# Kernel tuning notes

Measured on AMD Instinct MI355X. Metric: run time of the kernel, lower is better.

Reference implementation:

```python
import jax, jax.numpy as jnp
import numpy as np
import math

T = 120      # frame_num == audio_len == max_seq_len
D = 64       # hidden_layer_size
H = 2        # n_head
DH = D // H
DFF = 2 * D
DOUT = 31
PERIOD = 10
EPS = 1e-5
NEG = -1e9
SCALE = 1.0 / math.sqrt(DH)
SLOPES = (1.0 / 16.0, 1.0 / 256.0)  # ALiBi slopes for n_head=2


def _pe():
    # PeriodicPositionalEncoding: sinusoid over one period, tiled
    pos = jnp.arange(PERIOD, dtype=jnp.float32)[:, None]
    div = jnp.exp(jnp.arange(0, D, 2, dtype=jnp.float32) * (-math.log(10000.0) / D))
    s, c = jnp.sin(pos * div), jnp.cos(pos * div)
    pe = jnp.stack([s, c], axis=-1).reshape(PERIOD, D)  # interleave sin/cos
    return jnp.tile(pe, (T // PERIOD + 1, 1))[:T]


def _alibi_mask():
    # causal mask + ALiBi bias: alibi[i,j] = -slope * floor((i-j)/period) for j<=i
    slopes = jnp.array(SLOPES, dtype=jnp.float32)
    i = jnp.arange(T)[:, None]
    j = jnp.arange(T)[None, :]
    rel = ((i - j) // PERIOD).astype(jnp.float32)
    return jnp.where(j <= i, -slopes[:, None, None] * rel, NEG)  # [H,T,T]


def _ln(x, g, b):
    m = x.mean(-1, keepdims=True)
    v = ((x - m) ** 2).mean(-1, keepdims=True)
    return (x - m) / jnp.sqrt(v + EPS) * g + b


def setup_inputs() -> dict:
    key = jax.random.key(0)
    ks = iter(jax.random.split(key, 32))
    n = lambda shape, s=0.05: jax.random.normal(next(ks), shape, dtype=jnp.float32) * s
    inp = {
        'audio': jax.random.normal(next(ks), (1, T, 1024), dtype=jnp.float32),
        'W_audio': n((D, 1024)), 'b_audio': n((D,)),
        'obj_W': n((D, 5)),
        'Wq': n((D, D)), 'bq': n((D,)), 'Wk': n((D, D)), 'bk': n((D,)),
        'Wv': n((D, D)), 'bv': n((D,)), 'Wo': n((D, D)), 'bo': n((D,)),
        'Wv2': n((D, D)), 'bv2': n((D,)), 'Wo2': n((D, D)), 'bo2': n((D,)),
        'g1': jnp.ones((D,)), 'be1': jnp.zeros((D,)),
        'g2': jnp.ones((D,)), 'be2': jnp.zeros((D,)),
        'g3': jnp.ones((D,)), 'be3': jnp.zeros((D,)),
        'W1': n((DFF, D)), 'c1': n((DFF,)), 'W2': n((D, DFF)), 'c2': n((D,)),
        'Wr': n((DOUT, D)), 'br': n((DOUT,)), 'Wm': n((D, DOUT)), 'bm': n((D,)),
    }
    return inp


def _forward(audio, W_audio, b_audio, obj_W, Wq, bq, Wk, bk, Wv, bv, Wo, bo,
             Wv2, bv2, Wo2, bo2, g1, be1, g2, be2, g3, be3,
             W1, c1, W2, c2, Wr, br, Wm, bm):
    mem = audio[0] @ W_audio.T + b_audio          # [S,D], S == T
    style = obj_W[:, 0]                            # obj_vector @ [1,0,0,0,0]
    pe = _pe()
    mask = _alibi_mask()
    slopes = jnp.array(SLOPES, dtype=jnp.float32)
    jarr = jnp.arange(T)

    # enc_dec_mask leaves exactly one memory key per target row (anti-diagonal
    # from the end); the feedback row t at step t always attends memory[-1],
    # so its cross-attn output is just the projected value of the last frame.
    cross_last = (mem[-1] @ Wv2.T + bv2) @ Wo2.T + bo2  # [D]

    def step(emb, t):
        # decode only the last row (row t) of the growing sequence; 1-layer
        # post-norm decoder => row t depends only on input rows 0..t.
        x = emb + pe                                 # PPE over prefix
        xq = jnp.take(x, t, axis=0)                  # [D]
        q = (xq @ Wq.T + bq).reshape(H, DH)
        k = (x @ Wk.T + bk).reshape(T, H, DH)
        v = (x @ Wv.T + bv).reshape(T, H, DH)
        bias = jnp.where(jarr <= t,
                         -slopes[:, None] * ((t - jarr) // PERIOD).astype(jnp.float32),
                         NEG)                        # [H,T]
        sc = jnp.einsum('hd,shd->hs', q, k) * SCALE + bias
        a = jax.nn.softmax(sc, axis=-1)
        sa = jnp.einsum('hs,shd->hd', a, v).reshape(D) @ Wo.T + bo
        h1 = _ln(xq + sa, g1, be1)
        h2 = _ln(h1 + cross_last, g2, be2)
        h3 = _ln(h2 + jax.nn.relu(h2 @ W1.T + c1) @ W2.T + c2, g3, be3)
        new = (h3 @ Wr.T + br) @ Wm.T + bm + style   # vertice_map(vertice_map_r(.)) + style
        emb = jax.lax.dynamic_update_slice(emb, new[None, :], (t + 1, 0))
        return emb, None

    emb0 = jnp.zeros((T, D), audio.dtype).at[0].set(style)
    emb, _ = jax.lax.scan(step, emb0, jnp.arange(T - 1))

    # final full-length decode (last loop iteration of the torch module)
    x = emb + pe
    q = (x @ Wq.T + bq).reshape(T, H, DH)
    k = (x @ Wk.T + bk).reshape(T, H, DH)
    v = (x @ Wv.T + bv).reshape(T, H, DH)
    sc = jnp.einsum('thd,shd->hts', q, k) * SCALE + mask
    a = jax.nn.softmax(sc, axis=-1)
    sa = jnp.einsum('hts,shd->thd', a, v).reshape(T, D) @ Wo.T + bo
    h1 = _ln(x + sa, g1, be1)
    # at length T with S == T the enc_dec_mask aligns target row j <-> memory row j
    cross = (mem @ Wv2.T + bv2) @ Wo2.T + bo2
    h2 = _ln(h1 + cross, g2, be2)
    h3 = _ln(h2 + jax.nn.relu(h2 @ W1.T + c1) @ W2.T + c2, g3, be3)
    return (h3 @ Wr.T + br)[None]                    # [1,T,31]


def reference(audio, W_audio, b_audio, obj_W, Wq, bq, Wk, bk, Wv, bv, Wo, bo,
              Wv2, bv2, Wo2, bo2, g1, be1, g2, be2, g3, be3,
              W1, c1, W2, c2, Wr, br, Wm, bm):
    return _forward(audio, W_audio, b_audio, obj_W, Wq, bq, Wk, bk, Wv, bv, Wo, bo,
                    Wv2, bv2, Wo2, bo2, g1, be1, g2, be2, g3, be3,
                    W1, c1, W2, c2, Wr, br, Wm, bm)
```

## Files before the change

kernel.cpp:

```cpp
#include <hip/hip_runtime.h>

typedef unsigned short u16;
typedef unsigned int   u32;
typedef _Float16 f16;
typedef f16 h2 __attribute__((ext_vector_type(2)));
typedef f16 h4 __attribute__((ext_vector_type(4)));
typedef f16 h8 __attribute__((ext_vector_type(8)));

#define T_    120
#define D_    64
#define DOUT_ 31
#define KROW_ 68
#define VROW_ 132

#if defined(__has_builtin)
#if __has_builtin(__builtin_amdgcn_fdot2)
#define DOT2(a,b,c) __builtin_amdgcn_fdot2((a),(b),(c),false)
#endif
#endif
#ifndef DOT2
#define DOT2(a,b,c) ((float)(a).x*(float)(b).x + ((float)(a).y*(float)(b).y + (c)))
#endif
#define SHV(x,i,j) __builtin_shufflevector((x),(x),(i),(j))

__device__ __forceinline__ h2 pk(float a, float b){
#if defined(__has_builtin) && __has_builtin(__builtin_amdgcn_cvt_pkrtz)
  return __builtin_bit_cast(h2, __builtin_amdgcn_cvt_pkrtz(a, b));
#else
  h2 r; r.x = (f16)a; r.y = (f16)b; return r;
#endif
}
__device__ __forceinline__ float b2f(u16 u){ return __uint_as_float(((u32)u) << 16); }
__device__ __forceinline__ float2 bp2(u32 u){
  float2 r; r.x = __uint_as_float(u << 16); r.y = __uint_as_float(u & 0xffff0000u); return r;
}
__device__ __forceinline__ u16 f2bu(float f){
  u32 u = __float_as_uint(f);
  u32 r = u + 0x7fffu + ((u >> 16) & 1u);
  return (u16)(r >> 16);
}
__device__ __forceinline__ u16 f2h16(float x){
  f16 v = (f16)x; u16 r; __builtin_memcpy(&r, &v, 2); return r;
}
#define WSYNC() do{ __asm__ __volatile__("" ::: "memory"); __builtin_amdgcn_wave_barrier(); }while(0)

__device__ __forceinline__ float dpp_sum(float x){
  int t;
  t = __builtin_amdgcn_update_dpp(0, __float_as_int(x), 0x111, 0xf, 0xf, true); x += __int_as_float(t);
  t = __builtin_amdgcn_update_dpp(0, __float_as_int(x), 0x112, 0xf, 0xf, true); x += __int_as_float(t);
  t = __builtin_amdgcn_update_dpp(0, __float_as_int(x), 0x114, 0xf, 0xf, true); x += __int_as_float(t);
  t = __builtin_amdgcn_update_dpp(0, __float_as_int(x), 0x118, 0xf, 0xf, true); x += __int_as_float(t);
  t = __builtin_amdgcn_update_dpp(0, __float_as_int(x), 0x142, 0xf, 0xf, true); x += __int_as_float(t);
  t = __builtin_amdgcn_update_dpp(0, __float_as_int(x), 0x143, 0xf, 0xf, true); x += __int_as_float(t);
  return __int_as_float(__builtin_amdgcn_readlane(__float_as_int(x), 63));
}
__device__ __forceinline__ float dpp_max_pos(float x){
  int t;
  t = __builtin_amdgcn_update_dpp(0, __float_as_int(x), 0x111, 0xf, 0xf, true); x = fmaxf(x, __int_as_float(t));
  t = __builtin_amdgcn_update_dpp(0, __float_as_int(x), 0x112, 0xf, 0xf, true); x = fmaxf(x, __int_as_float(t));
  t = __builtin_amdgcn_update_dpp(0, __float_as_int(x), 0x114, 0xf, 0xf, true); x = fmaxf(x, __int_as_float(t));
  t = __builtin_amdgcn_update_dpp(0, __float_as_int(x), 0x118, 0xf, 0xf, true); x = fmaxf(x, __int_as_float(t));
  t = __builtin_amdgcn_update_dpp(0, __float_as_int(x), 0x142, 0xf, 0xf, true); x = fmaxf(x, __int_as_float(t));
  t = __builtin_amdgcn_update_dpp(0, __float_as_int(x), 0x143, 0xf, 0xf, true); x = fmaxf(x, __int_as_float(t));
  return __int_as_float(__builtin_amdgcn_readlane(__float_as_int(x), 63));
}
__device__ __forceinline__ float pe_val(int row, int i){
  const float coef = -0.28782313662425574f;
  int p = row % 10;
  float dv  = __expf((float)(i >> 1) * coef);
  float ang = (float)p * dv;
  return (i & 1) ? __cosf(ang) : __sinf(ang);
}
__device__ __forceinline__ void loadrow32(h2* dst, const float* row){
  #pragma unroll
  for (int r = 0; r < 16; ++r){
    float4 f = ((const float4*)row)[r];
    dst[2*r]   = pk(f.x, f.y);
    dst[2*r+1] = pk(f.z, f.w);
  }
}

__global__ __launch_bounds__(256) void k_pre(const float* __restrict__ audio,
                                             const float* __restrict__ Wa, const float* __restrict__ ba,
                                             const float* __restrict__ Wv2, const float* __restrict__ bv2,
                                             const float* __restrict__ Wo2, const float* __restrict__ bo2,
                                             const float* __restrict__ Wo, const float* __restrict__ W1,
                                             const float* __restrict__ W2, const float* __restrict__ Wr,
                                             const float* __restrict__ Wm, const float* __restrict__ br,
                                             const float* __restrict__ bm,
                                             float* __restrict__ cross, float* __restrict__ Ms,
                                             float* __restrict__ bMv,
                                             u16* __restrict__ wob, u16* __restrict__ w1b,
                                             u16* __restrict__ w2b, u16* __restrict__ wrb){
  const int b = blockIdx.x, tid = threadIdx.x;
  if (b == 120){
    for (int i = tid; i < 4096; i += 256) wob[i] = f2bu(Wo[i]);
    for (int i = tid; i < 8192; i += 256){ w1b[i] = f2bu(W1[i]); w2b[i] = f2bu(W2[i]); }
    for (int i = tid; i < 1984; i += 256) wrb[i] = f2bu(Wr[i]);
    for (int idx = tid; idx < 4096; idx += 256){
      int d = idx >> 6, e = idx & 63;
      float acc = 0.f;
      #pragma unroll
      for (int j = 0; j < 31; ++j) acc += Wm[d*31 + j] * Wr[j*64 + e];
      Ms[idx] = acc;
    }
    if (tid < 64){
      float acc = bm[tid];
      #pragma unroll
      for (int j = 0; j < 31; ++j) acc += Wm[tid*31 + j] * br[j];
      bMv[tid] = acc;
    }
    return;
  }
  __shared__ float ash[1024];
  __shared__ float msh[64], tsh[64];
  for (int i = tid; i < 1024; i += 256) ash[i] = audio[b*1024 + i];
  __syncthreads();
  const int w = tid >> 6, lane = tid & 63;
  for (int d = w*16; d < w*16 + 16; ++d){
    const float4* row = (const float4*)(Wa + d*1024);
    float acc = 0.f;
    #pragma unroll
    for (int m = 0; m < 4; ++m){
      float4 wp = row[lane + 64*m];
      int j = 4*(lane + 64*m);
      acc += wp.x*ash[j] + wp.y*ash[j+1] + wp.z*ash[j+2] + wp.w*ash[j+3];
    }
    acc = dpp_sum(acc);
    if (lane == 0) msh[d] = acc + ba[d];
  }
  __syncthreads();
  if (tid < 64){
    const float4* r1 = (const float4*)(Wv2 + tid*64);
    float a = bv2[tid];
    #pragma unroll
    for (int j = 0; j < 16; ++j){ float4 p = r1[j]; a += p.x*msh[4*j] + p.y*msh[4*j+1] + p.z*msh[4*j+2] + p.w*msh[4*j+3]; }
    tsh[tid] = a;
  }
  __syncthreads();
  if (tid < 64){
    const float4* r2 = (const float4*)(Wo2 + tid*64);
    float c = bo2[tid];
    #pragma unroll
    for (int j = 0; j < 16; ++j){ float4 p = r2[j]; c += p.x*tsh[4*j] + p.y*tsh[4*j+1] + p.z*tsh[4*j+2] + p.w*tsh[4*j+3]; }
    cross[b*64 + tid] = c;
  }
}

__global__ __launch_bounds__(128, 1) void k_scan(
    const float* __restrict__ objW,
    const float* __restrict__ Wq, const float* __restrict__ bq,
    const float* __restrict__ Wk, const float* __restrict__ bk,
    const float* __restrict__ Wv, const float* __restrict__ bv,
    const float* __restrict__ Wo, const float* __restrict__ bo,
    const float* __restrict__ g1, const float* __restrict__ be1,
    const float* __restrict__ g2, const float* __restrict__ be2,
    const float* __restrict__ g3, const float* __restrict__ be3,
    const float* __restrict__ W1, const float* __restrict__ c1,
    const float* __restrict__ W2, const float* __restrict__ c2,
    const float* __restrict__ Ms, const float* __restrict__ bMv,
    const float* __restrict__ cross,
    u16* __restrict__ xw16, u16* __restrict__ Kw16, u16* __restrict__ Vw16)
{
  __shared__ __align__(16) f16 KcS[128*KROW_];
  __shared__ __align__(16) f16 VcS[D_*VROW_];
  __shared__ __align__(16) f16 xwS[T_*D_];
  __shared__ __align__(16) f16 sch[256];
  __shared__ __align__(16) f16 xh[64], qh[64], ath[64], h2h[64], h3h[64];
  __shared__ __align__(16) h2  fsh2[64];
  __shared__ float xf[64], h2f[64];
  __shared__ float pe_tab[640];

  const int tid = threadIdx.x;
  const int i = tid & 63;
  const bool w0 = tid < 64;

  h2 R0[32], R1[32], R2[32], R3[32], R4[32];
  float bA=0.f, bB=0.f, c1a=0.f, c1b=0.f, c2r=0.f, bmst=0.f, cls_r=0.f;
  float g1r=0.f,b1r=0.f,g2r=0.f,b2r=0.f,g3r=0.f,b3r=0.f;

  if (w0){
    loadrow32(R0, Wv + i*64);
    loadrow32(R1, Wo + i*64);
    loadrow32(R2, W1 + i*64);
    loadrow32(R3, W1 + (64+i)*64);
    bA = bv[i]; bB = bo[i]; c1a = c1[i]; c1b = c1[64+i];
    g1r = g1[i]; b1r = be1[i]; g2r = g2[i]; b2r = be2[i];
    cls_r = cross[119*64 + i];
  } else {
    loadrow32(R0, Wq + i*64);
    loadrow32(R1, Wk + i*64);
    {
      const float4* ra = (const float4*)(W2 + i*128);
      const float4* rb = (const float4*)(W2 + i*128 + 64);
      #pragma unroll
      for (int r = 0; r < 8; ++r){
        float4 a = ra[r], b = rb[r];
        R2[4*r+0] = pk(a.x, b.x); R2[4*r+1] = pk(a.y, b.y);
        R2[4*r+2] = pk(a.z, b.z); R2[4*r+3] = pk(a.w, b.w);
      }
      #pragma unroll
      for (int r = 0; r < 8; ++r){
        float4 a = ra[8+r], b = rb[8+r];
        R3[4*r+0] = pk(a.x, b.x); R3[4*r+1] = pk(a.y, b.y);
        R3[4*r+2] = pk(a.z, b.z); R3[4*r+3] = pk(a.w, b.w);
      }
    }
    loadrow32(R4, Ms + i*64);
    bA = bq[i]; bB = bk[i]; c2r = c2[i];
    g3r = g3[i]; b3r = be3[i];
    bmst = bMv[i] + objW[i*5];
  }
  { u32* p = (u32*)KcS; for (int idx = tid; idx < 128*KROW_/2; idx += 128) p[idx] = 0; }
  { u32* p = (u32*)VcS; for (int idx = tid; idx < D_*VROW_/2;  idx += 128) p[idx] = 0; }
  for (int idx = tid; idx < 640; idx += 128) pe_tab[idx] = pe_val(idx >> 6, idx & 63);
  __syncthreads();

  if (!w0){
    float st = objW[i*5];
    float x0 = st + pe_val(0, i);
    xf[i] = x0; xh[i] = (f16)x0; xwS[i] = (f16)x0;
    WSYNC();
    const h8* xv = (const h8*)xh;
    float q0=bA,q1=0.f,q2=0.f,q3=0.f, k0=bB,k1=0.f,k2=0.f,k3=0.f;
    #pragma unroll
    for (int r = 0; r < 8; ++r){
      h8 x = xv[r];
      h2 xa=SHV(x,0,1), xb=SHV(x,2,3), xc=SHV(x,4,5), xd=SHV(x,6,7);
      q0 = DOT2(R0[4*r+0], xa, q0); q1 = DOT2(R0[4*r+1], xb, q1);
      q2 = DOT2(R0[4*r+2], xc, q2); q3 = DOT2(R0[4*r+3], xd, q3);
      k0 = DOT2(R1[4*r+0], xa, k0); k1 = DOT2(R1[4*r+1], xb, k1);
      k2 = DOT2(R1[4*r+2], xc, k2); k3 = DOT2(R1[4*r+3], xd, k3);
    }
    qh[i] = (f16)((q0+q1)+(q2+q3));
    KcS[i] = (f16)((k0+k1)+(k2+k3));
  }

  int pp = 1;
  for (int t = 0; t < T_-1; ++t){
    __syncthreads();
    if (w0){
      {
        const h8* xv = (const h8*)xh;
        float v0=bA,v1=0.f,v2=0.f,v3=0.f;
        #pragma unroll
        for (int r = 0; r < 8; ++r){
          h8 x = xv[r];
          v0 = DOT2(R0[4*r+0], SHV(x,0,1), v0);
          v1 = DOT2(R0[4*r+1], SHV(x,2,3), v1);
          v2 = DOT2(R0[4*r+2], SHV(x,4,5), v2);
          v3 = DOT2(R0[4*r+3], SHV(x,6,7), v3);
        }
        VcS[i*VROW_ + t] = (f16)((v0+v1)+(v2+v3));
      }
      WSYNC();
      {
        const h8* qv  = (const h8*)qh;
        const h4* kr0 = (const h4*)(KcS + i*KROW_);
        const h4* kr1 = (const h4*)(KcS + (i+64)*KROW_);
        float d00a=0.f,d00b=0.f,d01a=0.f,d01b=0.f,d10a=0.f,d10b=0.f,d11a=0.f,d11b=0.f;
        #pragma unroll
        for (int r = 0; r < 4; ++r){
          h8 ql = qv[r], qhn = qv[4+r];
          h2 ql0=SHV(ql,0,1),  ql1=SHV(ql,2,3),  ql2=SHV(ql,4,5),  ql3=SHV(ql,6,7);
          h2 qh0=SHV(qhn,0,1), qh1=SHV(qhn,2,3), qh2=SHV(qhn,4,5), qh3=SHV(qhn,6,7);
          h4 ka = kr0[2*r],   kb = kr0[2*r+1];
          h4 kc = kr0[8+2*r], kd = kr0[9+2*r];
          h4 ke = kr1[2*r],   kf = kr1[2*r+1];
          h4 kg = kr1[8+2*r], kh = kr1[9+2*r];
          d00a = DOT2(SHV(ka,0,1), ql0, d00a); d00b = DOT2(SHV(ka,2,3), ql1, d00b);
          d00a = DOT2(SHV(kb,0,1), ql2, d00a); d00b = DOT2(SHV(kb,2,3), ql3, d00b);
          d10a = DOT2(SHV(kc,0,1), qh0, d10a); d10b = DOT2(SHV(kc,2,3), qh1, d10b);
          d10a = DOT2(SHV(kd,0,1), qh2, d10a); d10b = DOT2(SHV(kd,2,3), qh3, d10b);
          d01a = DOT2(SHV(ke,0,1), ql0, d01a); d01b = DOT2(SHV(ke,2,3), ql1, d01b);
          d01a = DOT2(SHV(kf,0,1), ql2, d01a); d01b = DOT2(SHV(kf,2,3), ql3, d01b);
          d11a = DOT2(SHV(kg,0,1), qh0, d11a); d11b = DOT2(SHV(kg,2,3), qh1, d11b);
          d11a = DOT2(SHV(kh,0,1), qh2, d11a); d11b = DOT2(SHV(kh,2,3), qh3, d11b);
        }
        const float SC = 0.17677669529663687f;
        int r0 = (t - i) / 10, r1 = (t - i - 64) / 10;
        bool m0 = (i <= t), m1 = (i + 64 <= t);
        float e00 = m0 ? __expf((d00a+d00b)*SC - 0.0625f*(float)r0)     : 0.f;
        float e01 = m1 ? __expf((d01a+d01b)*SC - 0.0625f*(float)r1)     : 0.f;
        float e10 = m0 ? __expf((d10a+d10b)*SC - 0.00390625f*(float)r0) : 0.f;
        float e11 = m1 ? __expf((d11a+d11b)*SC - 0.00390625f*(float)r1) : 0.f;
        float inv0 = 1.f / dpp_sum(e00 + e01);
        float inv1 = 1.f / dpp_sum(e10 + e11);
        sch[i]        = (f16)(e00*inv0);
        sch[64+i]     = (f16)(e01*inv0);
        sch[128+i]    = (f16)(e10*inv1);
        sch[192+i]    = (f16)(e11*inv1);
      }
      WSYNC();
      {
        const h8* av = (const h8*)(sch + (i >> 5)*128);
        const h4* vv = (const h4*)(VcS + i*VROW_);
        float p0=0.f,p1=0.f,p2=0.f,p3=0.f;
        #pragma unroll
        for (int r = 0; r < 15; ++r){
          h8 a = av[r];
          h4 va = vv[2*r], vb = vv[2*r+1];
          p0 = DOT2(SHV(va,0,1), SHV(a,0,1), p0);
          p1 = DOT2(SHV(va,2,3), SHV(a,2,3), p1);
          p2 = DOT2(SHV(vb,0,1), SHV(a,4,5), p2);
          p3 = DOT2(SHV(vb,2,3), SHV(a,6,7), p3);
        }
        ath[i] = (f16)((p0+p1)+(p2+p3));
      }
      WSYNC();
      {
        const h8* av = (const h8*)ath;
        float a0=bB, a1=0.f, a2=0.f, a3=0.f;
        #pragma unroll
        for (int r = 0; r < 8; ++r){
          h8 x = av[r];
          a0 = DOT2(R1[4*r+0], SHV(x,0,1), a0);
          a1 = DOT2(R1[4*r+1], SHV(x,2,3), a1);
          a2 = DOT2(R1[4*r+2], SHV(x,4,5), a2);
          a3 = DOT2(R1[4*r+3], SHV(x,6,7), a3);
        }
        float y = xf[i] + (a0+a1)+(a2+a3);
        float s = dpp_sum(y), s2 = dpp_sum(y*y);
        float m = s*(1.f/64.f), var = fmaxf(s2*(1.f/64.f) - m*m, 0.f);
        float h1 = (y - m)*rsqrtf(var + 1e-5f)*g1r + b1r;
        float z = h1 + cls_r;
        float sz = dpp_sum(z), sz2 = dpp_sum(z*z);
        float mz = sz*(1.f/64.f), vz = fmaxf(sz2*(1.f/64.f) - mz*mz, 0.f);
        float h2v = (z - mz)*rsqrtf(vz + 1e-5f)*g2r + b2r;
        h2h[i] = (f16)h2v;
        h2f[i] = h2v;
      }
      WSYNC();
      {
        const h8* hv = (const h8*)h2h;
        float a0=c1a, a1=0.f, a2=0.f, a3=0.f, b0=c1b, b1=0.f, b2=0.f, b3=0.f;
        #pragma unroll
        for (int r = 0; r < 8; ++r){
          h8 x = hv[r];
          h2 xa=SHV(x,0,1), xb=SHV(x,2,3), xc=SHV(x,4,5), xd=SHV(x,6,7);
          a0 = DOT2(R2[4*r+0], xa, a0); a1 = DOT2(R2[4*r+1], xb, a1);
          a2 = DOT2(R2[4*r+2], xc, a2); a3 = DOT2(R2[4*r+3], xd, a3);
          b0 = DOT2(R3[4*r+0], xa, b0); b1 = DOT2(R3[4*r+1], xb, b1);
          b2 = DOT2(R3[4*r+2], xc, b2); b3 = DOT2(R3[4*r+3], xd, b3);
        }
        fsh2[i] = pk(fmaxf((a0+a1)+(a2+a3), 0.f), fmaxf((b0+b1)+(b2+b3), 0.f));
      }
    }
    __syncthreads();
    if (!w0){
      float h3v;
      {
        const h8* fv = (const h8*)fsh2;
        float a0=c2r, a1=0.f, a2=0.f, a3=0.f;
        #pragma unroll
        for (int r = 0; r < 8; ++r){
          h8 x = fv[r];
          a0 = DOT2(R2[4*r+0], SHV(x,0,1), a0);
          a1 = DOT2(R2[4*r+1], SHV(x,2,3), a1);
          a2 = DOT2(R2[4*r+2], SHV(x,4,5), a2);
          a3 = DOT2(R2[4*r+3], SHV(x,6,7), a3);
        }
        #pragma unroll
        for (int r = 0; r < 8; ++r){
          h8 x = fv[8+r];
          a0 = DOT2(R3[4*r+0], SHV(x,0,1), a0);
          a1 = DOT2(R3[4*r+1], SHV(x,2,3), a1);
          a2 = DOT2(R3[4*r+2], SHV(x,4,5), a2);
          a3 = DOT2(R3[4*r+3], SHV(x,6,7), a3);
        }
        float y = h2f[i] + (a0+a1)+(a2+a3);
        float s = dpp_sum(y), s2 = dpp_sum(y*y);
        float m = s*(1.f/64.f), var = fmaxf(s2*(1.f/64.f) - m*m, 0.f);
        h3v = (y - m)*rsqrtf(var + 1e-5f)*g3r + b3r;
        h3h[i] = (f16)h3v;
      }
      WSYNC();
      {
        const h8* hv3 = (const h8*)h3h;
        float m0=bmst, m1=0.f, m2=0.f, m3=0.f;
        #pragma unroll
        for (int r = 0; r < 8; ++r){
          h8 x = hv3[r];
          m0 = DOT2(R4[4*r+0], SHV(x,0,1), m0);
          m1 = DOT2(R4[4*r+1], SHV(x,2,3), m1);
          m2 = DOT2(R4[4*r+2], SHV(x,4,5), m2);
          m3 = DOT2(R4[4*r+3], SHV(x,6,7), m3);
        }
        float xn = (m0+m1)+(m2+m3) + pe_tab[pp*64 + i];
        xf[i] = xn;
        xh[i] = (f16)xn;
        xwS[(t+1)*64 + i] = (f16)xn;
      }
      WSYNC();
      {
        const h8* xv = (const h8*)xh;
        float q0=bA,q1=0.f,q2=0.f,q3=0.f, k0=bB,k1=0.f,k2=0.f,k3=0.f;
        #pragma unroll
        for (int r = 0; r < 8; ++r){
          h8 x = xv[r];
          h2 xa=SHV(x,0,1), xb=SHV(x,2,3), xc=SHV(x,4,5), xd=SHV(x,6,7);
          q0 = DOT2(R0[4*r+0], xa, q0); q1 = DOT2(R0[4*r+1], xb, q1);
          q2 = DOT2(R0[4*r+2], xc, q2); q3 = DOT2(R0[4*r+3], xd, q3);
          k0 = DOT2(R1[4*r+0], xa, k0); k1 = DOT2(R1[4*r+1], xb, k1);
          k2 = DOT2(R1[4*r+2], xc, k2); k3 = DOT2(R1[4*r+3], xd, k3);
        }
        qh[i] = (f16)((q0+q1)+(q2+q3));
        KcS[(t+1)*KROW_ + i] = (f16)((k0+k1)+(k2+k3));
      }
    }
    pp = (pp == 9) ? 0 : pp + 1;
  }
  __syncthreads();
  if (w0){
    const h8* xv = (const h8*)xh;
    float v0=bA,v1=0.f,v2=0.f,v3=0.f;
    #pragma unroll
    for (int r = 0; r < 8; ++r){
      h8 x = xv[r];
      v0 = DOT2(R0[4*r+0], SHV(x,0,1), v0);
      v1 = DOT2(R0[4*r+1], SHV(x,2,3), v1);
      v2 = DOT2(R0[4*r+2], SHV(x,4,5), v2);
      v3 = DOT2(R0[4*r+3], SHV(x,6,7), v3);
    }
    Vw16[119*64 + i] = f2h16((v0+v1)+(v2+v3));
  }
  {
    const u16* kc = (const u16*)KcS;
    const u16* vc = (const u16*)VcS;
    for (int idx = tid; idx < 120*64; idx += 128){
      int t_ = idx >> 6, d = idx & 63;
      Kw16[idx] = kc[t_*KROW_ + d];
    }
    for (int idx = tid; idx < 119*64; idx += 128){
      int t_ = idx >> 6, d = idx & 63;
      Vw16[idx] = vc[d*VROW_ + t_];
    }
    const u32* xs32 = (const u32*)xwS;
    for (int idx = tid; idx < T_*D_/2; idx += 128) ((u32*)xw16)[idx] = xs32[idx];
  }
}

__global__ __launch_bounds__(128) void k_final(
    const float* __restrict__ Wq, const float* __restrict__ bq, const float* __restrict__ bo,
    const float* __restrict__ g1, const float* __restrict__ be1,
    const float* __restrict__ g2, const float* __restrict__ be2,
    const float* __restrict__ g3, const float* __restrict__ be3,
    const float* __restrict__ c1, const float* __restrict__ c2, const float* __restrict__ br,
    const u16* __restrict__ wo_b, const u16* __restrict__ w1_b,
    const u16* __restrict__ w2_b, const u16* __restrict__ wr_b,
    const float* __restrict__ cross, const u16* __restrict__ xw16,
    const u16* __restrict__ Kw16, const u16* __restrict__ Vw16,
    float* __restrict__ out)
{
  __shared__ float xs[64], qs[64], at[64], h2s[64], h3s[64], fs[128], sc[256];
  const int irow = blockIdx.x, tid = threadIdx.x;
  const f16* xp = (const f16*)xw16;
  const f16* kp = (const f16*)Kw16;
  const f16* vp = (const f16*)Vw16;
  if (tid < 64) xs[tid] = (float)xp[irow*64 + tid];
  __syncthreads();
  if (tid < 64){
// ... 105 lines not shown
  const float* Wo   =(const float*)d_in[10];
  const float* bo   =(const float*)d_in[11];
  const float* Wv2  =(const float*)d_in[12];
  const float* bv2  =(const float*)d_in[13];
  const float* Wo2  =(const float*)d_in[14];
  const float* bo2  =(const float*)d_in[15];
  const float* g1   =(const float*)d_in[16];
  const float* be1  =(const float*)d_in[17];
  const float* g2   =(const float*)d_in[18];
  const float* be2  =(const float*)d_in[19];
  const float* g3   =(const float*)d_in[20];
  const float* be3  =(const float*)d_in[21];
  const float* W1   =(const float*)d_in[22];
  const float* c1   =(const float*)d_in[23];
  const float* W2   =(const float*)d_in[24];
  const float* c2   =(const float*)d_in[25];
  const float* Wr   =(const float*)d_in[26];
  const float* br   =(const float*)d_in[27];
  const float* Wm   =(const float*)d_in[28];
  const float* bm   =(const float*)d_in[29];

  float* ws    = (float*)d_ws;
  float* cross = ws;
  float* Ms    = ws + 7680;
  float* bMv   = ws + 11776;
  u16* xw16 = (u16*)(ws + 11840);
  u16* Kw16 = xw16 + 7680;
  u16* Vw16 = Kw16 + 7680;
  u16* wo_b = Vw16 + 7680;
  u16* w1_b = wo_b + 4096;
  u16* w2_b = w1_b + 8192;
  u16* wr_b = w2_b + 8192;
  float* out = (float*)d_out;

  k_pre  <<<dim3(121), dim3(256), 0, stream>>>(audio, Wa, ba, Wv2, bv2, Wo2, bo2,
                                               Wo, W1, W2, Wr, Wm, br, bm,
                                               cross, Ms, bMv, wo_b, w1_b, w2_b, wr_b);
  k_scan <<<dim3(1),   dim3(128), 0, stream>>>(objW, Wq, bq, Wk, bk, Wv, bv, Wo, bo,
                                               g1, be1, g2, be2, g3, be3,
                                               W1, c1, W2, c2, Ms, bMv,
                                               cross, xw16, Kw16, Vw16);
  k_final<<<dim3(120), dim3(128), 0, stream>>>(Wq, bq, bo, g1, be1, g2, be2, g3, be3,
                                               c1, c2, br, wo_b, w1_b, w2_b, wr_b,
                                               cross, xw16, Kw16, Vw16, out);
}
```

Measured before the change: 411.4 us.

## Fold output-map into QKV weights and run scan as single wave

Precomputes the composed matrices Wq·M, Wk·M, Wv·M and the per-phase bias vectors (including positional encoding) in the prep kernel. The serial scan can then produce next q/k/v/x directly from h3 in one fused matvec stage instead of computing x and then projecting it. The scan drops from two waves with __syncthreads to a single 64-thread wave using only wave barriers, with some weights moved from registers to LDS. The aim is to shorten the serial per-step dependency chain and remove block-level sync, at the cost of more precompute in the prep kernel, LDS weight reads and small fp16 rounding differences.

After: 563.9 us. 37.1% more time.

```diff
diff --git a/kernel.cpp b/kernel.cpp
--- a/kernel.cpp
+++ b/kernel.cpp
@@ -12,6 +12,7 @@
 #define DOUT_ 31
 #define KROW_ 68
 #define VROW_ 132
+#define WP_   68
 
 #if defined(__has_builtin)
 #if __has_builtin(__builtin_amdgcn_fdot2)
@@ -30,7 +31,6 @@
   h2 r; r.x = (f16)a; r.y = (f16)b; return r;
 #endif
 }
-__device__ __forceinline__ float b2f(u16 u){ return __uint_as_float(((u32)u) << 16); }
 __device__ __forceinline__ float2 bp2(u32 u){
   float2 r; r.x = __uint_as_float(u << 16); r.y = __uint_as_float(u & 0xffff0000u); return r;
 }
@@ -38,9 +38,6 @@
   u32 u = __float_as_uint(f);
   u32 r = u + 0x7fffu + ((u >> 16) & 1u);
   return (u16)(r >> 16);
-}
-__device__ __forceinline__ u16 f2h16(float x){
-  f16 v = (f16)x; u16 r; __builtin_memcpy(&r, &v, 2); return r;
 }
 #define WSYNC() do{ __asm__ __volatile__("" ::: "memory"); __builtin_amdgcn_wave_barrier(); }while(0)
 
@@ -87,13 +84,25 @@
                                              const float* __restrict__ Wo, const float* __restrict__ W1,
                                              const float* __restrict__ W2, const float* __restrict__ Wr,
                                              const float* __restrict__ Wm, const float* __restrict__ br,
-                                             const float* __restrict__ bm,
-                                             float* __restrict__ cross, float* __restrict__ Ms,
-                                             float* __restrict__ bMv,
+                                             const float* __restrict__ bm, const float* __restrict__ objW,
+                                             const float* __restrict__ Wq, const float* __restrict__ bq,
+                                             const float* __restrict__ Wk, const float* __restrict__ bk,
+                                             const float* __restrict__ Wv, const float* __restrict__ bv,
+                                             float* __restrict__ cross,
+                                             float* __restrict__ Mw,  float* __restrict__ QMw,
+                                             float* __restrict__ KMw, float* __restrict__ VMw,
+                                             float* __restrict__ qbw, float* __restrict__ kbw,
+                                             float* __restrict__ vbw, float* __restrict__ xbw,
+                                             float* __restrict__ q0w, float* __restrict__ k0w,
+                                             float* __restrict__ v0w, float* __restrict__ x0w,
                                              u16* __restrict__ wob, u16* __restrict__ w1b,
                                              u16* __restrict__ w2b, u16* __restrict__ wrb){
   const int b = blockIdx.x, tid = threadIdx.x;
   if (b == 120){
+    __shared__ float Msh[4096];
+    __shared__ float bMs[64];
+    __shared__ float uS[640];
+    __shared__ float x0s[64];
     for (int i = tid; i < 4096; i += 256) wob[i] = f2bu(Wo[i]);
     for (int i = tid; i < 8192; i += 256){ w1b[i] = f2bu(W1[i]); w2b[i] = f2bu(W2[i]); }
     for (int i = tid; i < 1984; i += 256) wrb[i] = f2bu(Wr[i]);
@@ -102,13 +111,50 @@
       float acc = 0.f;
       #pragma unroll
       for (int j = 0; j < 31; ++j) acc += Wm[d*31 + j] * Wr[j*64 + e];
-      Ms[idx] = acc;
+      Msh[idx] = acc; Mw[idx] = acc;
     }
     if (tid < 64){
       float acc = bm[tid];
       #pragma unroll
       for (int j = 0; j < 31; ++j) acc += Wm[tid*31 + j] * br[j];
-      bMv[tid] = acc;
+      bMs[tid] = acc + objW[tid*5];
+      x0s[tid] = objW[tid*5] + pe_val(0, tid);
+    }
+    __syncthreads();
+    for (int idx = tid; idx < 640; idx += 256){
+      int p = idx >> 6, d = idx & 63;
+      float u = bMs[d] + pe_val(p, d);
+      uS[idx] = u; xbw[idx] = u;
+    }
+    __syncthreads();
+    for (int idx = tid; idx < 4096; idx += 256){
+      int d = idx >> 6, e = idx & 63;
+      float aq = 0.f, ak = 0.f, av = 0.f;
+      #pragma unroll
+      for (int j = 0; j < 64; ++j){
+        float m = Msh[j*64 + e];
+        aq += Wq[d*64 + j]*m; ak += Wk[d*64 + j]*m; av += Wv[d*64 + j]*m;
+      }
+      QMw[idx] = aq; KMw[idx] = ak; VMw[idx] = av;
+    }
+    for (int idx = tid; idx < 640; idx += 256){
+      int p = idx >> 6, d = idx & 63;
+      float aq = bq[d], ak = bk[d], av = bv[d];
+      #pragma unroll
+      for (int j = 0; j < 64; ++j){
+        float u = uS[p*64 + j];
+        aq += Wq[d*64 + j]*u; ak += Wk[d*64 + j]*u; av += Wv[d*64 + j]*u;
+      }
+      qbw[idx] = aq; kbw[idx] = ak; vbw[idx] = av;
+    }
+    if (tid < 64){
+      float aq = bq[tid], ak = bk[tid], av = bv[tid];
+      #pragma unroll
+      for (int j = 0; j < 64; ++j){
+        float x = x0s[j];
+        aq += Wq[tid*64 + j]*x; ak += Wk[tid*64 + j]*x; av += Wv[tid*64 + j]*x;
+      }
+      q0w[tid] = aq; k0w[tid] = ak; v0w[tid] = av; x0w[tid] = x0s[tid];
     }
     return;
   }
@@ -147,296 +193,235 @@
   }
 }
 
-__global__ __launch_bounds__(128, 1) void k_scan(
-    const float* __restrict__ objW,
-    const float* __restrict__ Wq, const float* __restrict__ bq,
-    const float* __restrict__ Wk, const float* __restrict__ bk,
-    const float* __restrict__ Wv, const float* __restrict__ bv,
+__global__ __launch_bounds__(64, 1) void k_scan(
     const float* __restrict__ Wo, const float* __restrict__ bo,
+    const float* __restrict__ W1, const float* __restrict__ c1,
+    const float* __restrict__ W2, const float* __restrict__ c2,
     const float* __restrict__ g1, const float* __restrict__ be1,
     const float* __restrict__ g2, const float* __restrict__ be2,
     const float* __restrict__ g3, const float* __restrict__ be3,
-    const float* __restrict__ W1, const float* __restrict__ c1,
-    const float* __restrict__ W2, const float* __restrict__ c2,
-    const float* __restrict__ Ms, const float* __restrict__ bMv,
+    const float* __restrict__ Mw,  const float* __restrict__ QMw,
+    const float* __restrict__ KMw, const float* __restrict__ VMw,
+    const float* __restrict__ qbw, const float* __restrict__ kbw,
+    const float* __restrict__ vbw, const float* __restrict__ xbw,
+    const float* __restrict__ q0w, const float* __restrict__ k0w,
+    const float* __restrict__ v0w, const float* __restrict__ x0w,
     const float* __restrict__ cross,
     u16* __restrict__ xw16, u16* __restrict__ Kw16, u16* __restrict__ Vw16)
 {
   __shared__ __align__(16) f16 KcS[128*KROW_];
   __shared__ __align__(16) f16 VcS[D_*VROW_];
   __shared__ __align__(16) f16 xwS[T_*D_];
+  __shared__ __align__(16) f16 W1bS[D_*WP_];
+  __shared__ __align__(16) f16 W2aS[D_*WP_];
+  __shared__ __align__(16) f16 W2bS[D_*WP_];
+  __shared__ __align__(16) f16 MS[D_*WP_];
+  __shared__ float qbS[640], kbS[640], vbS[640], xbS[640];
   __shared__ __align__(16) f16 sch[256];
-  __shared__ __align__(16) f16 xh[64], qh[64], ath[64], h2h[64], h3h[64];
-  __shared__ __align__(16) h2  fsh2[64];
-  __shared__ float xf[64], h2f[64];
-  __shared__ float pe_tab[640];
-
-  const int tid = threadIdx.x;
-  const int i = tid & 63;
-  const bool w0 = tid < 64;
-
-  h2 R0[32], R1[32], R2[32], R3[32], R4[32];
-  float bA=0.f, bB=0.f, c1a=0.f, c1b=0.f, c2r=0.f, bmst=0.f, cls_r=0.f;
-  float g1r=0.f,b1r=0.f,g2r=0.f,b2r=0.f,g3r=0.f,b3r=0.f;
-
-  if (w0){
-    loadrow32(R0, Wv + i*64);
-    loadrow32(R1, Wo + i*64);
-    loadrow32(R2, W1 + i*64);
-    loadrow32(R3, W1 + (64+i)*64);
-    bA = bv[i]; bB = bo[i]; c1a = c1[i]; c1b = c1[64+i];
-    g1r = g1[i]; b1r = be1[i]; g2r = g2[i]; b2r = be2[i];
-    cls_r = cross[119*64 + i];
-  } else {
-    loadrow32(R0, Wq + i*64);
-    loadrow32(R1, Wk + i*64);
-    {
-      const float4* ra = (const float4*)(W2 + i*128);
-      const float4* rb = (const float4*)(W2 + i*128 + 64);
-      #pragma unroll
-      for (int r = 0; r < 8; ++r){
-        float4 a = ra[r], b = rb[r];
-        R2[4*r+0] = pk(a.x, b.x); R2[4*r+1] = pk(a.y, b.y);
-        R2[4*r+2] = pk(a.z, b.z); R2[4*r+3] = pk(a.w, b.w);
-      }
-      #pragma unroll
-      for (int r = 0; r < 8; ++r){
-        float4 a = ra[8+r], b = rb[8+r];
-        R3[4*r+0] = pk(a.x, b.x); R3[4*r+1] = pk(a.y, b.y);
-        R3[4*r+2] = pk(a.z, b.z); R3[4*r+3] = pk(a.w, b.w);
-      }
-    }
-    loadrow32(R4, Ms + i*64);
-    bA = bq[i]; bB = bk[i]; c2r = c2[i];
-    g3r = g3[i]; b3r = be3[i];
-    bmst = bMv[i] + objW[i*5];
-  }
-  { u32* p = (u32*)KcS; for (int idx = tid; idx < 128*KROW_/2; idx += 128) p[idx] = 0; }
-  { u32* p = (u32*)VcS; for (int idx = tid; idx < D_*VROW_/2;  idx += 128) p[idx] = 0; }
-  for (int idx = tid; idx < 640; idx += 128) pe_tab[idx] = pe_val(idx >> 6, idx & 63);
-  __syncthreads();
-
-  if (!w0){
-    float st = objW[i*5];
-    float x0 = st + pe_val(0, i);
-    xf[i] = x0; xh[i] = (f16)x0; xwS[i] = (f16)x0;
-    WSYNC();
-    const h8* xv = (const h8*)xh;
-    float q0=bA,q1=0.f,q2=0.f,q3=0.f, k0=bB,k1=0.f,k2=0.f,k3=0.f;
-    #pragma unroll
-    for (int r = 0; r < 8; ++r){
-      h8 x = xv[r];
-      h2 xa=SHV(x,0,1), xb=SHV(x,2,3), xc=SHV(x,4,5), xd=SHV(x,6,7);
-      q0 = DOT2(R0[4*r+0], xa, q0); q1 = DOT2(R0[4*r+1], xb, q1);
-      q2 = DOT2(R0[4*r+2], xc, q2); q3 = DOT2(R0[4*r+3], xd, q3);
-      k0 = DOT2(R1[4*r+0], xa, k0); k1 = DOT2(R1[4*r+1], xb, k1);
-      k2 = DOT2(R1[4*r+2], xc, k2); k3 = DOT2(R1[4*r+3], xd, k3);
-    }
-    qh[i] = (f16)((q0+q1)+(q2+q3));
-    KcS[i] = (f16)((k0+k1)+(k2+k3));
-  }
+  __shared__ __align__(16) f16 qh[64], ath[64], h2h[64], h3h[64];
+  __shared__ __align__(16) f16 fsh[128];
+
+  const int i = threadIdx.x;
+
+  h2 QM[32], KM[32], VM[32], WOr[32], W1a[32];
+  loadrow32(QM,  QMw + i*64);
+  loadrow32(KM,  KMw + i*64);
+  loadrow32(VM,  VMw + i*64);
+  loadrow32(WOr, Wo  + i*64);
+  loadrow32(W1a, W1  + i*64);
+  const float bo_r = bo[i], c1a = c1[i], c1b = c1[64+i], c2r = c2[i];
+  const float g1r = g1[i], b1r = be1[i], g2r = g2[i], b2r = be2[i], g3r = g3[i], b3r = be3[i];
+  const float cls_r = cross[119*64 + i];
+
+  for (int idx = i; idx < 4096; idx += 64){
+    int r = idx >> 6, c = idx & 63;
+    W1bS[r*WP_ + c] = (f16)W1[(64+r)*64 + c];
+    W2aS[r*WP_ + c] = (f16)W2[r*128 + c];
+    W2bS[r*WP_ + c] = (f16)W2[r*128 + 64 + c];
+    MS  [r*WP_ + c] = (f16)Mw[r*64 + c];
+  }
+  for (int idx = i; idx < 640; idx += 64){
+    qbS[idx] = qbw[idx]; kbS[idx] = kbw[idx]; vbS[idx] = vbw[idx]; xbS[idx] = xbw[idx];
+  }
+  { u32* p = (u32*)KcS; for (int idx = i; idx < 128*KROW_/2; idx += 64) p[idx] = 0; }
+  { u32* p = (u32*)VcS; for (int idx = i; idx < D_*VROW_/2;  idx += 64) p[idx] = 0; }
+  float xr = x0w[i];
+  qh[i] = (f16)q0w[i];
+  KcS[i] = (f16)k0w[i];
+  VcS[i*VROW_] = (f16)v0w[i];
+  xwS[i] = (f16)xr;
+  WSYNC();
 
   int pp = 1;
   for (int t = 0; t < T_-1; ++t){
-    __syncthreads();
-    if (w0){
-      {
-        const h8* xv = (const h8*)xh;
-        float v0=bA,v1=0.f,v2=0.f,v3=0.f;
-        #pragma unroll
-        for (int r = 0; r < 8; ++r){
-          h8 x = xv[r];
-          v0 = DOT2(R0[4*r+0], SHV(x,0,1), v0);
-          v1 = DOT2(R0[4*r+1], SHV(x,2,3), v1);
-          v2 = DOT2(R0[4*r+2], SHV(x,4,5), v2);
-          v3 = DOT2(R0[4*r+3], SHV(x,6,7), v3);
-        }
-        VcS[i*VROW_ + t] = (f16)((v0+v1)+(v2+v3));
-      }
-      WSYNC();
-      {
-        const h8* qv  = (const h8*)qh;
-        const h4* kr0 = (const h4*)(KcS + i*KROW_);
-        const h4* kr1 = (const h4*)(KcS + (i+64)*KROW_);
-        float d00a=0.f,d00b=0.f,d01a=0.f,d01b=0.f,d10a=0.f,d10b=0.f,d11a=0.f,d11b=0.f;
-        #pragma unroll
-        for (int r = 0; r < 4; ++r){
-          h8 ql = qv[r], qhn = qv[4+r];
-          h2 ql0=SHV(ql,0,1),  ql1=SHV(ql,2,3),  ql2=SHV(ql,4,5),  ql3=SHV(ql,6,7);
-          h2 qh0=SHV(qhn,0,1), qh1=SHV(qhn,2,3), qh2=SHV(qhn,4,5), qh3=SHV(qhn,6,7);
-          h4 ka = kr0[2*r],   kb = kr0[2*r+1];
-          h4 kc = kr0[8+2*r], kd = kr0[9+2*r];
-          h4 ke = kr1[2*r],   kf = kr1[2*r+1];
-          h4 kg = kr1[8+2*r], kh = kr1[9+2*r];
-          d00a = DOT2(SHV(ka,0,1), ql0, d00a); d00b = DOT2(SHV(ka,2,3), ql1, d00b);
-          d00a = DOT2(SHV(kb,0,1), ql2, d00a); d00b = DOT2(SHV(kb,2,3), ql3, d00b);
-          d10a = DOT2(SHV(kc,0,1), qh0, d10a); d10b = DOT2(SHV(kc,2,3), qh1, d10b);
-          d10a = DOT2(SHV(kd,0,1), qh2, d10a); d10b = DOT2(SHV(kd,2,3), qh3, d10b);
-          d01a = DOT2(SHV(ke,0,1), ql0, d01a); d01b = DOT2(SHV(ke,2,3), ql1, d01b);
-          d01a = DOT2(SHV(kf,0,1), ql2, d01a); d01b = DOT2(SHV(kf,2,3), ql3, d01b);
-          d11a = DOT2(SHV(kg,0,1), qh0, d11a); d11b = DOT2(SHV(kg,2,3), qh1, d11b);
-          d11a = DOT2(SHV(kh,0,1), qh2, d11a); d11b = DOT2(SHV(kh,2,3), qh3, d11b);
-        }
-        const float SC = 0.17677669529663687f;
-        int r0 = (t - i) / 10, r1 = (t - i - 64) / 10;
-        bool m0 = (i <= t), m1 = (i + 64 <= t);
-        float e00 = m0 ? __expf((d00a+d00b)*SC - 0.0625f*(float)r0)     : 0.f;
-        float e01 = m1 ? __expf((d01a+d01b)*SC - 0.0625f*(float)r1)     : 0.f;
-        float e10 = m0 ? __expf((d10a+d10b)*SC - 0.00390625f*(float)r0) : 0.f;
-        float e11 = m1 ? __expf((d11a+d11b)*SC - 0.00390625f*(float)r1) : 0.f;
-        float inv0 = 1.f / dpp_sum(e00 + e01);
-        float inv1 = 1.f / dpp_sum(e10 + e11);
-        sch[i]        = (f16)(e00*inv0);
-        sch[64+i]     = (f16)(e01*inv0);
-        sch[128+i]    = (f16)(e10*inv1);
-        sch[192+i]    = (f16)(e11*inv1);
-      }
-      WSYNC();
-      {
-        const h8* av = (const h8*)(sch + (i >> 5)*128);
-        const h4* vv = (const h4*)(VcS + i*VROW_);
-        float p0=0.f,p1=0.f,p2=0.f,p3=0.f;
-        #pragma unroll
-        for (int r = 0; r < 15; ++r){
-          h8 a = av[r];
-          h4 va = vv[2*r], vb = vv[2*r+1];
-          p0 = DOT2(SHV(va,0,1), SHV(a,0,1), p0);
-          p1 = DOT2(SHV(va,2,3), SHV(a,2,3), p1);
-          p2 = DOT2(SHV(vb,0,1), SHV(a,4,5), p2);
-          p3 = DOT2(SHV(vb,2,3), SHV(a,6,7), p3);
-        }
-        ath[i] = (f16)((p0+p1)+(p2+p3));
-      }
-      WSYNC();
-      {
-        const h8* av = (const h8*)ath;
-        float a0=bB, a1=0.f, a2=0.f, a3=0.f;
-        #pragma unroll
-        for (int r = 0; r < 8; ++r){
-          h8 x = av[r];
-          a0 = DOT2(R1[4*r+0], SHV(x,0,1), a0);
-          a1 = DOT2(R1[4*r+1], SHV(x,2,3), a1);
-          a2 = DOT2(R1[4*r+2], SHV(x,4,5), a2);
-          a3 = DOT2(R1[4*r+3], SHV(x,6,7), a3);
-        }
-        float y = xf[i] + (a0+a1)+(a2+a3);
-        float s = dpp_sum(y), s2 = dpp_sum(y*y);
-        float m = s*(1.f/64.f), var = fmaxf(s2*(1.f/64.f) - m*m, 0.f);
-        float h1 = (y - m)*rsqrtf(var + 1e-5f)*g1r + b1r;
-        float z = h1 + cls_r;
-        float sz = dpp_sum(z), sz2 = dpp_sum(z*z);
-        float mz = sz*(1.f/64.f), vz = fmaxf(sz2*(1.f/64.f) - mz*mz, 0.f);
-        float h2v = (z - mz)*rsqrtf(vz + 1e-5f)*g2r + b2r;
-        h2h[i] = (f16)h2v;
-        h2f[i] = h2v;
-      }
-      WSYNC();
-      {
-        const h8* hv = (const h8*)h2h;
-        float a0=c1a, a1=0.f, a2=0.f, a3=0.f, b0=c1b, b1=0.f, b2=0.f, b3=0.f;
-        #pragma unroll
-        for (int r = 0; r < 8; ++r){
-          h8 x = hv[r];
-          h2 xa=SHV(x,0,1), xb=SHV(x,2,3), xc=SHV(x,4,5), xd=SHV(x,6,7);
-          a0 = DOT2(R2[4*r+0], xa, a0); a1 = DOT2(R2[4*r+1], xb, a1);
-          a2 = DOT2(R2[4*r+2], xc, a2); a3 = DOT2(R2[4*r+3], xd, a3);
-          b0 = DOT2(R3[4*r+0], xa, b0); b1 = DOT2(R3[4*r+1], xb, b1);
-          b2 = DOT2(R3[4*r+2], xc, b2); b3 = DOT2(R3[4*r+3], xd, b3);
-        }
-        fsh2[i] = pk(fmaxf((a0+a1)+(a2+a3), 0.f), fmaxf((b0+b1)+(b2+b3), 0.f));
-      }
-    }
-    __syncthreads();
-    if (!w0){
-      float h3v;
-      {
-        const h8* fv = (const h8*)fsh2;
-        float a0=c2r, a1=0.f, a2=0.f, a3=0.f;
-        #pragma unroll
-        for (int r = 0; r < 8; ++r){
-          h8 x = fv[r];
-          a0 = DOT2(R2[4*r+0], SHV(x,0,1), a0);
-          a1 = DOT2(R2[4*r+1], SHV(x,2,3), a1);
-          a2 = DOT2(R2[4*r+2], SHV(x,4,5), a2);
-          a3 = DOT2(R2[4*r+3], SHV(x,6,7), a3);
-        }
-        #pragma unroll
-        for (int r = 0; r < 8; ++r){
-          h8 x = fv[8+r];
-          a0 = DOT2(R3[4*r+0], SHV(x,0,1), a0);
-          a1 = DOT2(R3[4*r+1], SHV(x,2,3), a1);
-          a2 = DOT2(R3[4*r+2], SHV(x,4,5), a2);
-          a3 = DOT2(R3[4*r+3], SHV(x,6,7), a3);
-        }
-        float y = h2f[i] + (a0+a1)+(a2+a3);
-        float s = dpp_sum(y), s2 = dpp_sum(y*y);
-        float m = s*(1.f/64.f), var = fmaxf(s2*(1.f/64.f) - m*m, 0.f);
-        h3v = (y - m)*rsqrtf(var + 1e-5f)*g3r + b3r;
-        h3h[i] = (f16)h3v;
-      }
-      WSYNC();
-      {
-        const h8* hv3 = (const h8*)h3h;
-        float m0=bmst, m1=0.f, m2=0.f, m3=0.f;
-        #pragma unroll
-        for (int r = 0; r < 8; ++r){
-          h8 x = hv3[r];
-          m0 = DOT2(R4[4*r+0], SHV(x,0,1), m0);
-          m1 = DOT2(R4[4*r+1], SHV(x,2,3), m1);
-          m2 = DOT2(R4[4*r+2], SHV(x,4,5), m2);
-          m3 = DOT2(R4[4*r+3], SHV(x,6,7), m3);
-        }
-        float xn = (m0+m1)+(m2+m3) + pe_tab[pp*64 + i];
-        xf[i] = xn;
-        xh[i] = (f16)xn;
-        xwS[(t+1)*64 + i] = (f16)xn;
-      }
-      WSYNC();
-      {
-        const h8* xv = (const h8*)xh;
-        float q0=bA,q1=0.f,q2=0.f,q3=0.f, k0=bB,k1=0.f,k2=0.f,k3=0.f;
-        #pragma unroll
-        for (int r = 0; r < 8; ++r){
-          h8 x = xv[r];
-          h2 xa=SHV(x,0,1), xb=SHV(x,2,3), xc=SHV(x,4,5), xd=SHV(x,6,7);
-          q0 = DOT2(R0[4*r+0], xa, q0); q1 = DOT2(R0[4*r+1], xb, q1);
-          q2 = DOT2(R0[4*r+2], xc, q2); q3 = DOT2(R0[4*r+3], xd, q3);
-          k0 = DOT2(R1[4*r+0], xa, k0); k1 = DOT2(R1[4*r+1], xb, k1);
-          k2 = DOT2(R1[4*r+2], xc, k2); k3 = DOT2(R1[4*r+3], xd, k3);
-        }
-        qh[i] = (f16)((q0+q1)+(q2+q3));
-        KcS[(t+1)*KROW_ + i] = (f16)((k0+k1)+(k2+k3));
-      }
-    }
+    {
+      const h8* qv  = (const h8*)qh;
+      const h4* kr0 = (const h4*)(KcS + i*KROW_);
+      const h4* kr1 = (const h4*)(KcS + (i+64)*KROW_);
+      float d00a=0.f,d00b=0.f,d01a=0.f,d01b=0.f,d10a=0.f,d10b=0.f,d11a=0.f,d11b=0.f;
+      #pragma unroll
+      for (int r = 0; r < 4; ++r){
+        h8 ql = qv[r], qhn = qv[4+r];
+        h2 ql0=SHV(ql,0,1),  ql1=SHV(ql,2,3),  ql2=SHV(ql,4,5),  ql3=SHV(ql,6,7);
+        h2 qh0=SHV(qhn,0,1), qh1=SHV(qhn,2,3), qh2=SHV(qhn,4,5), qh3=SHV(qhn,6,7);
+        h4 ka = kr0[2*r],   kb = kr0[2*r+1];
+        h4 kc = kr0[8+2*r], kd = kr0[9+2*r];
+        h4 ke = kr1[2*r],   kf = kr1[2*r+1];
+        h4 kg = kr1[8+2*r], kh = kr1[9+2*r];
+        d00a = DOT2(SHV(ka,0,1), ql0, d00a); d00b = DOT2(SHV(ka,2,3), ql1, d00b);
+        d00a = DOT2(SHV(kb,0,1), ql2, d00a); d00b = DOT2(SHV(kb,2,3), ql3, d00b);
+        d10a = DOT2(SHV(kc,0,1), qh0, d10a); d10b = DOT2(SHV(kc,2,3), qh1, d10b);
+        d10a = DOT2(SHV(kd,0,1), qh2, d10a); d10b = DOT2(SHV(kd,2,3), qh3, d10b);
+        d01a = DOT2(SHV(ke,0,1), ql0, d01a); d01b = DOT2(SHV(ke,2,3), ql1, d01b);
+        d01a = DOT2(SHV(kf,0,1), ql2, d01a); d01b = DOT2(SHV(kf,2,3), ql3, d01b);
+        d11a = DOT2(SHV(kg,0,1), qh0, d11a); d11b = DOT2(SHV(kg,2,3), qh1, d11b);
+        d11a = DOT2(SHV(kh,0,1), qh2, d11a); d11b = DOT2(SHV(kh,2,3), qh3, d11b);
+      }
+      const float SC = 0.17677669529663687f;
+      int r0 = (t - i) / 10, r1 = (t - i - 64) / 10;
+      bool m0 = (i <= t), m1 = (i + 64 <= t);
+      float e00 = m0 ? __expf((d00a+d00b)*SC - 0.0625f*(float)r0)     : 0.f;
+      float e01 = m1 ? __expf((d01a+d01b)*SC - 0.0625f*(float)r1)     : 0.f;
+      float e10 = m0 ? __expf((d10a+d10b)*SC - 0.00390625f*(float)r0) : 0.f;
+      float e11 = m1 ? __expf((d11a+d11b)*SC - 0.00390625f*(float)r1) : 0.f;
+      float inv0 = 1.f / dpp_sum(e00 + e01);
+      float inv1 = 1.f / dpp_sum(e10 + e11);
+      sch[i]      = (f16)(e00*inv0);
+      sch[64+i]   = (f16)(e01*inv0);
+      sch[128+i]  = (f16)(e10*inv1);
+      sch[192+i]  = (f16)(e11*inv1);
+    }
+    WSYNC();
+    {
+      const h8* av = (const h8*)(sch + (i >> 5)*128);
+      const h4* vv = (const h4*)(VcS + i*VROW_);
+      float p0=0.f,p1=0.f,p2=0.f,p3=0.f;
+      #pragma unroll
+      for (int r = 0; r < 15; ++r){
+        h8 a = av[r];
+        h4 va = vv[2*r], vb = vv[2*r+1];
+        p0 = DOT2(SHV(va,0,1), SHV(a,0,1), p0);
+        p1 = DOT2(SHV(va,2,3), SHV(a,2,3), p1);
+        p2 = DOT2(SHV(vb,0,1), SHV(a,4,5), p2);
+        p3 = DOT2(SHV(vb,2,3), SHV(a,6,7), p3);
+      }
+      ath[i] = (f16)((p0+p1)+(p2+p3));
+    }
+    WSYNC();
+    float h2v;
+    {
+      const h8* av = (const h8*)ath;
+      float a0=bo_r, a1=0.f, a2=0.f, a3=0.f;
+      #pragma unroll
+      for (int r = 0; r < 8; ++r){
+        h8 x = av[r];
+        a0 = DOT2(WOr[4*r+0], SHV(x,0,1), a0);
+        a1 = DOT2(WOr[4*r+1], SHV(x,2,3), a1);
+        a2 = DOT2(WOr[4*r+2], SHV(x,4,5), a2);
+        a3 = DOT2(WOr[4*r+3], SHV(x,6,7), a3);
+      }
+      float y = xr + (a0+a1)+(a2+a3);
+      float s = dpp_sum(y), s2 = dpp_sum(y*y);
+      float m = s*(1.f/64.f), var = fmaxf(s2*(1.f/64.f) - m*m, 0.f);
+      float h1 = (y - m)*rsqrtf(var + 1e-5f)*g1r + b1r;
+      float z = h1 + cls_r;
+      float sz = dpp_sum(z), sz2 = dpp_sum(z*z);
+      float mz = sz*(1.f/64.f), vz = fmaxf(sz2*(1.f/64.f) - mz*mz, 0.f);
+      h2v = (z - mz)*rsqrtf(vz + 1e-5f)*g2r + b2r;
+      h2h[i] = (f16)h2v;
+    }
+    WSYNC();
+    {
+      const h8* hv = (const h8*)h2h;
+      const h4* w1b_ = (const h4*)(W1bS + i*WP_);
+      float a0=c1a, a1=0.f, a2=0.f, a3=0.f, b0=c1b, b1=0.f, b2=0.f, b3=0.f;
+      #pragma unroll
+      for (int r = 0; r < 8; ++r){
+        h8 x = hv[r];
+        h2 xa=SHV(x,0,1), xb=SHV(x,2,3), xc=SHV(x,4,5), xd=SHV(x,6,7);
+        a0 = DOT2(W1a[4*r+0], xa, a0); a1 = DOT2(W1a[4*r+1], xb, a1);
+        a2 = DOT2(W1a[4*r+2], xc, a2); a3 = DOT2(W1a[4*r+3], xd, a3);
+        h4 wa = w1b_[2*r], wb = w1b_[2*r+1];
+        b0 = DOT2(SHV(wa,0,1), xa, b0); b1 = DOT2(SHV(wa,2,3), xb, b1);
+        b2 = DOT2(SHV(wb,0,1), xc, b2); b3 = DOT2(SHV(wb,2,3), xd, b3);
+      }
+      fsh[i]    = (f16)fmaxf((a0+a1)+(a2+a3), 0.f);
+      fsh[64+i] = (f16)fmaxf((b0+b1)+(b2+b3), 0.f);
+    }
+    WSYNC();
+    float h3v;
+    {
+      const h8* fv = (const h8*)fsh;
+      const h4* wa_ = (const h4*)(W2aS + i*WP_);
+      const h4* wb_ = (const h4*)(W2bS + i*WP_);
+      float a0=c2r, a1=0.f, a2=0.f, a3=0.f;
+      #pragma unroll
+      for (int r = 0; r < 8; ++r){
+        h8 x = fv[r];
+        h4 p = wa_[2*r], q = wa_[2*r+1];
+        a0 = DOT2(SHV(p,0,1), SHV(x,0,1), a0);
+        a1 = DOT2(SHV(p,2,3), SHV(x,2,3), a1);
+        a2 = DOT2(SHV(q,0,1), SHV(x,4,5), a2);
+        a3 = DOT2(SHV(q,2,3), SHV(x,6,7), a3);
+      }
+      #pragma unroll
+      for (int r = 0; r < 8; ++r){
+        h8 x = fv[8+r];
+        h4 p = wb_[2*r], q = wb_[2*r+1];
+        a0 = DOT2(SHV(p,0,1), SHV(x,0,1), a0);
+        a1 = DOT2(SHV(p,2,3), SHV(x,2,3), a1);
+        a2 = DOT2(SHV(q,0,1), SHV(x,4,5), a2);
+        a3 = DOT2(SHV(q,2,3), SHV(x,6,7), a3);
+      }
+      float y = h2v + (a0+a1)+(a2+a3);
+      float s = dpp_sum(y), s2 = dpp_sum(y*y);
+      float m = s*(1.f/64.f), var = fmaxf(s2*(1.f/64.f) - m*m, 0.f);
+      h3v = (y - m)*rsqrtf(var + 1e-5f)*g3r + b3r;
+      h3h[i] = (f16)h3v;
+    }
+    WSYNC();
+    {
+      const h8* hv3 = (const h8*)h3h;
+      const h4* mr_ = (const h4*)(MS + i*WP_);
+      float q0=qbS[pp*64+i], q1=0.f, q2=0.f, q3=0.f;
+      float k0=kbS[pp*64+i], k1=0.f, k2=0.f, k3=0.f;
+      float v0=vbS[pp*64+i], v1=0.f, v2=0.f, v3=0.f;
+      float x0=xbS[pp*64+i], x1=0.f, x2=0.f, x3=0.f;
+      #pragma unroll
+      for (int r = 0; r < 8; ++r){
+        h8 x = hv3[r];
+        h2 xa=SHV(x,0,1), xb=SHV(x,2,3), xc=SHV(x,4,5), xd=SHV(x,6,7);
+        q0 = DOT2(QM[4*r+0], xa, q0); q1 = DOT2(QM[4*r+1], xb, q1);
+        q2 = DOT2(QM[4*r+2], xc, q2); q3 = DOT2(QM[4*r+3], xd, q3);
+        k0 = DOT2(KM[4*r+0], xa, k0); k1 = DOT2(KM[4*r+1], xb, k1);
+        k2 = DOT2(KM[4*r+2], xc, k2); k3 = DOT2(KM[4*r+3], xd, k3);
+        v0 = DOT2(VM[4*r+0], xa, v0); v1 = DOT2(VM[4*r+1], xb, v1);
+        v2 = DOT2(VM[4*r+2], xc, v2); v3 = DOT2(VM[4*r+3], xd, v3);
+        h4 ma = mr_[2*r], mb = mr_[2*r+1];
+        x0 = DOT2(SHV(ma,0,1), xa, x0); x1 = DOT2(SHV(ma,2,3), xb, x1);
+        x2 = DOT2(SHV(mb,0,1), xc, x2); x3 = DOT2(SHV(mb,2,3), xd, x3);
+      }
+      float qv_ = (q0+q1)+(q2+q3), kv_ = (k0+k1)+(k2+k3);
+      float vv_ = (v0+v1)+(v2+v3), xv_ = (x0+x1)+(x2+x3);
+      qh[i] = (f16)qv_;
+      KcS[(t+1)*KROW_ + i] = (f16)kv_;
+      VcS[i*VROW_ + (t+1)] = (f16)vv_;
+      xr = xv_;
+      xwS[(t+1)*64 + i] = (f16)xv_;
+    }
+    WSYNC();
     pp = (pp == 9) ? 0 : pp + 1;
-  }
-  __syncthreads();
-  if (w0){
-    const h8* xv = (const h8*)xh;
-    float v0=bA,v1=0.f,v2=0.f,v3=0.f;
-    #pragma unroll
-    for (int r = 0; r < 8; ++r){
-      h8 x = xv[r];
-      v0 = DOT2(R0[4*r+0], SHV(x,0,1), v0);
-      v1 = DOT2(R0[4*r+1], SHV(x,2,3), v1);
-      v2 = DOT2(R0[4*r+2], SHV(x,4,5), v2);
-      v3 = DOT2(R0[4*r+3], SHV(x,6,7), v3);
-    }
-    Vw16[119*64 + i] = f2h16((v0+v1)+(v2+v3));
   }
   {
     const u16* kc = (const u16*)KcS;
     const u16* vc = (const u16*)VcS;
-    for (int idx = tid; idx < 120*64; idx += 128){
+    for (int idx = i; idx < 120*64; idx += 64){
       int t_ = idx >> 6, d = idx & 63;
       Kw16[idx] = kc[t_*KROW_ + d];
-    }
-    for (int idx = tid; idx < 119*64; idx += 128){
-      int t_ = idx >> 6, d = idx & 63;
       Vw16[idx] = vc[d*VROW_ + t_];
     }
     const u32* xs32 = (const u32*)xwS;
-    for (int idx = tid; idx < T_*D_/2; idx += 128) ((u32*)xw16)[idx] = xs32[idx];
+    for (int idx = i; idx < T_*D_/2; idx += 64) ((u32*)xw16)[idx] = xs32[idx];
   }
 }
 
@@ -588,9 +573,19 @@
 
   float* ws    = (float*)d_ws;
   float* cross = ws;
-  float* Ms    = ws + 7680;
-  float* bMv   = ws + 11776;
-  u16* xw16 = (u16*)(ws + 11840);
+  float* Mw    = ws + 7680;
+  float* QMw   = ws + 11776;
+  float* KMw   = ws + 15872;
+  float* VMw   = ws + 19968;
+  float* qbw   = ws + 24064;
+  float* kbw   = ws + 24704;
+  float* vbw   = ws + 25344;
+  float* xbw   = ws + 25984;
+  float* q0w   = ws + 26624;
+  float* k0w   = ws + 26688;
+  float* v0w   = ws + 26752;
+  float* x0w   = ws + 26816;
+  u16* xw16 = (u16*)(ws + 26880);
   u16* Kw16 = xw16 + 7680;
   u16* Vw16 = Kw16 + 7680;
   u16* wo_b = Vw16 + 7680;
@@ -600,11 +595,15 @@
   float* out = (float*)d_out;
 
   k_pre  <<<dim3(121), dim3(256), 0, stream>>>(audio, Wa, ba, Wv2, bv2, Wo2, bo2,
-                                               Wo, W1, W2, Wr, Wm, br, bm,
-                                               cross, Ms, bMv, wo_b, w1_b, w2_b, wr_b);
-  k_scan <<<dim3(1),   dim3(128), 0, stream>>>(objW, Wq, bq, Wk, bk, Wv, bv, Wo, bo,
+                                               Wo, W1, W2, Wr, Wm, br, bm, objW,
+                                               Wq, bq, Wk, bk, Wv, bv,
+                                               cross, Mw, QMw, KMw, VMw,
+                                               qbw, kbw, vbw, xbw, q0w, k0w, v0w, x0w,
+                                               wo_b, w1_b, w2_b, wr_b);
+  k_scan <<<dim3(1),   dim3(64),  0, stream>>>(Wo, bo, W1, c1, W2, c2,
                                                g1, be1, g2, be2, g3, be3,
-                                               W1, c1, W2, c2, Ms, bMv,
+                                               Mw, QMw, KMw, VMw, qbw, kbw, vbw, xbw,
+                                               q0w, k0w, v0w, x0w,
                                                cross, xw16, Kw16, Vw16);
   k_final<<<dim3(120), dim3(128), 0, stream>>>(Wq, bq, bo, g1, be1, g2, be2, g3, be3,
                                                c1, c2, br, wo_b, w1_b, w2_b, wr_b,
```
